# Kernel optimization log

Hardware: AMD Instinct MI355X
Metric: run time of the kernel (lower is better)

The kernel has to match this reference:

```python
import jax, jax.numpy as jnp
import numpy as np

HEAD_DIM = 64
NUM_FEATURES = 256


def _sample_orf(head_dim, num_features, seed=0):
    """Orthogonal random features with chi(d)-norm row scaling (FAVOR+)."""
    rng = np.random.RandomState(seed)
    blocks = []
    while len(blocks) * head_dim < num_features:
        G = rng.randn(head_dim, head_dim).astype(np.float32)
        Q, _ = np.linalg.qr(G)
        norms = np.linalg.norm(rng.randn(head_dim, head_dim).astype(np.float32), axis=1)
        blocks.append(np.diag(norms) @ Q.T)
    return np.concatenate(blocks, axis=0)[:num_features].astype(np.float32)


def _phi(x, omega, is_query):
    """FAVOR+ positive feature map with max-subtraction stabilization."""
    m = omega.shape[0]
    proj = jnp.einsum('bhnd,md->bhnm', x, omega)          # [B,H,N,M]
    norm = 0.5 * jnp.sum(x * x, axis=-1, keepdims=True)    # [B,H,N,1]
    log_phi = proj - norm
    if is_query:
        log_phi = log_phi - jnp.max(log_phi, axis=-1, keepdims=True)
    else:
        log_phi = log_phi - jnp.max(log_phi)
    return jnp.exp(log_phi) / np.float32(np.sqrt(m)) + 1e-4


def _causal_scan(phi_q, phi_k, v):
    """Causal linear-attention recurrence via lax.scan. States: S[B,H,M,D], z[B,H,M]."""
    B, H, N, M = phi_q.shape
    D = v.shape[-1]
    # seq-first for scan: [N,B,H,*]
    pq = jnp.moveaxis(phi_q, 2, 0)
    pk = jnp.moveaxis(phi_k, 2, 0)
    vt = jnp.moveaxis(v, 2, 0)

    S0 = jnp.zeros((B, H, M, D), dtype=phi_q.dtype)
    z0 = jnp.zeros((B, H, M), dtype=phi_q.dtype)

    def step(carry, xs):
        S, z = carry
        pq_i, pk_i, v_i = xs  # [B,H,M], [B,H,M], [B,H,D]
        S = S + pk_i[..., :, None] * v_i[..., None, :]
        z = z + pk_i
        num = jnp.einsum('bhm,bhmd->bhd', pq_i, S)
        den = jnp.sum(pq_i * z, axis=-1, keepdims=True) + 1e-6
        return (S, z), num / den

    _, out = jax.lax.scan(step, (S0, z0), (pq, pk, vt))  # out: [N,B,H,D]
    return jnp.moveaxis(out, 0, 2)


def setup_inputs() -> dict:
    key = jax.random.key(0)
    k1, k2, k3 = jax.random.split(key, 3)
    B, H, N, D = 2, 16, 4096, HEAD_DIM
    q = jax.random.normal(k1, (B, H, N, D), dtype=jnp.float32)
    k = jax.random.normal(k2, (B, H, N, D), dtype=jnp.float32)
    v = jax.random.normal(k3, (B, H, N, D), dtype=jnp.float32)
    omega = jnp.asarray(_sample_orf(HEAD_DIM, NUM_FEATURES))
    return {"q": q, "k": k, "v": v, "omega": omega}


def reference(q, k, v, omega):
    scale = q.shape[-1] ** (-0.25)
    phi_q = _phi(q * scale, omega, is_query=True)
    phi_k = _phi(k * scale, omega, is_query=False)
    # q_len == kv_len -> causal scan branch (matches original forward)
    out = _causal_scan(phi_q.astype(jnp.float32), phi_k.astype(jnp.float32),
                       v.astype(jnp.float32))
    return out.astype(q.dtype)
```

## Files before the change

kernel.cpp:

```cpp
#include <hip/hip_runtime.h>
#include <cstddef>

#define BH    32
#define NSEQ  4096
#define MFEAT 256
#define CHUNK 128
#define NCH   32
#define SROW  65
#define SPITCH (SROW*256)

#define SCALE 0.35355339059327373f

typedef unsigned int uint_t;
typedef _Float16 half_t;
typedef __attribute__((ext_vector_type(8))) _Float16 half8;
typedef __attribute__((ext_vector_type(4))) float f32x4;

__device__ __forceinline__ f32x4 mfma16(half8 a, half8 b, f32x4 c) {
  return __builtin_amdgcn_mfma_f32_16x16x32_f16(a, b, c, 0, 0, 0);
}
__device__ __forceinline__ uint_t enc_f(float x) {
  uint_t u = __float_as_uint(x);
  return (u & 0x80000000u) ? ~u : (u | 0x80000000u);
}
__device__ __forceinline__ float dec_f(uint_t u) {
  u = (u & 0x80000000u) ? (u ^ 0x80000000u) : ~u;
  return __uint_as_float(u);
}
__device__ __forceinline__ half8 cvt_h8(float4 a, float4 b) {
  half8 h;
  h[0] = (half_t)a.x; h[1] = (half_t)a.y; h[2] = (half_t)a.z; h[3] = (half_t)a.w;
  h[4] = (half_t)b.x; h[5] = (half_t)b.y; h[6] = (half_t)b.z; h[7] = (half_t)b.w;
  return h;
}

__global__ void k_init(uint_t* kmax) { *kmax = enc_f(-__builtin_inff()); }

__global__ __launch_bounds__(256, 2) void k_phi1(
    const float* __restrict__ q, const float* __restrict__ kx,
    const float* __restrict__ omega, uint_t* __restrict__ kmax,
    half_t* __restrict__ phiQ, float* __restrict__ hnKg)
{
  __shared__ half_t Wl[256 * 64];
  __shared__ float nrm[64];
  __shared__ float red[4];

  const int tid = threadIdx.x;
  const int lane = tid & 63;
  const int w = tid >> 6;
  const int lc = lane & 15, rg = lane >> 4, koff = rg * 8;
  const int swz = (lc & 7) << 3;
  const bool qpath = (blockIdx.x < 2048);
  const size_t rowbase = (size_t)(qpath ? blockIdx.x : (blockIdx.x - 2048)) * 64;

  for (int l = tid; l < 2048; l += 256) {
    int m = l >> 3, d8 = (l & 7) * 8;
    float4 a = *(const float4*)(omega + m * 64 + d8);
    float4 b = *(const float4*)(omega + m * 64 + d8 + 4);
    *(half8*)&Wl[m * 64 + (d8 ^ ((m & 7) << 3))] = cvt_h8(a, b);
  }

  if (qpath) {
    half8 aq[2];
    {
      const float* qp = q + (rowbase + w * 16 + lc) * 64 + koff;
      #pragma unroll
      for (int ks = 0; ks < 2; ks++) {
        float4 a = *(const float4*)(qp + ks * 32);
        float4 b = *(const float4*)(qp + ks * 32 + 4);
        a.x *= SCALE; a.y *= SCALE; a.z *= SCALE; a.w *= SCALE;
        b.x *= SCALE; b.y *= SCALE; b.z *= SCALE; b.w *= SCALE;
        aq[ks] = cvt_h8(a, b);
      }
    }
    __syncthreads();
    f32x4 acc[16];
    #pragma unroll
    for (int ct = 0; ct < 16; ct++) acc[ct] = (f32x4){0.f, 0.f, 0.f, 0.f};
    #pragma unroll
    for (int ks = 0; ks < 2; ks++)
      #pragma unroll
      for (int ct = 0; ct < 16; ct++) {
        half8 b = *(const half8*)&Wl[(ct * 16 + lc) * 64 + ((ks * 32 + koff) ^ swz)];
        acc[ct] = mfma16(aq[ks], b, acc[ct]);
      }
    float rowm[4];
    #pragma unroll
    for (int r = 0; r < 4; r++) {
      float m0 = -3.4e38f;
      #pragma unroll
      for (int ct = 0; ct < 16; ct++) m0 = fmaxf(m0, acc[ct][r]);
      m0 = fmaxf(m0, __shfl_xor(m0, 1, 64));
      m0 = fmaxf(m0, __shfl_xor(m0, 2, 64));
      m0 = fmaxf(m0, __shfl_xor(m0, 4, 64));
      m0 = fmaxf(m0, __shfl_xor(m0, 8, 64));
      rowm[r] = m0;
    }
    #pragma unroll
    for (int ct = 0; ct < 16; ct++)
      #pragma unroll
      for (int r = 0; r < 4; r++)
        acc[ct][r] = __expf(acc[ct][r] - rowm[r]) * 0.0625f + 1e-4f;

    half_t* st = Wl;
    #pragma unroll
    for (int hh = 0; hh < 2; hh++) {
      __syncthreads();
      #pragma unroll
      for (int c8 = 0; c8 < 8; c8++)
        #pragma unroll
        for (int r = 0; r < 4; r++)
          st[(w * 16 + rg * 4 + r) * 136 + c8 * 16 + lc] = (half_t)acc[hh * 8 + c8][r];
      __syncthreads();
      #pragma unroll
      for (int e = 0; e < 4; e++) {
        int l = tid + e * 256;
        int row = l >> 4, c = (l & 15) * 8;
        *(half8*)(phiQ + (rowbase + row) * 256 + hh * 128 + c) =
            *(const half8*)&st[row * 136 + c];
      }
    }
  } else {
    half8 akf[2];
    {
      const float* kp = kx + (rowbase + w * 16 + lc) * 64 + koff;
      float pn = 0.f;
      #pragma unroll
      for (int ks = 0; ks < 2; ks++) {
        float4 c = *(const float4*)(kp + ks * 32);
        float4 d = *(const float4*)(kp + ks * 32 + 4);
        c.x *= SCALE; c.y *= SCALE; c.z *= SCALE; c.w *= SCALE;
        d.x *= SCALE; d.y *= SCALE; d.z *= SCALE; d.w *= SCALE;
        pn += c.x * c.x + c.y * c.y + c.z * c.z + c.w * c.w
            + d.x * d.x + d.y * d.y + d.z * d.z + d.w * d.w;
        akf[ks] = cvt_h8(c, d);
      }
      pn += __shfl_xor(pn, 16, 64);
      pn += __shfl_xor(pn, 32, 64);
      if (rg == 0) {
        nrm[w * 16 + lc] = 0.5f * pn;
        hnKg[rowbase + w * 16 + lc] = 0.5f * pn;
      }
    }
    __syncthreads();
    f32x4 acc[16];
    #pragma unroll
    for (int ct = 0; ct < 16; ct++) acc[ct] = (f32x4){0.f, 0.f, 0.f, 0.f};
    #pragma unroll
    for (int ks = 0; ks < 2; ks++)
      #pragma unroll
      for (int ct = 0; ct < 16; ct++) {
        half8 b = *(const half8*)&Wl[(ct * 16 + lc) * 64 + ((ks * 32 + koff) ^ swz)];
        acc[ct] = mfma16(akf[ks], b, acc[ct]);
      }
    float hn[4];
    #pragma unroll
    for (int r = 0; r < 4; r++) hn[r] = nrm[w * 16 + rg * 4 + r];
    float bm = -3.4e38f;
    #pragma unroll
    for (int ct = 0; ct < 16; ct++)
      #pragma unroll
      for (int r = 0; r < 4; r++) bm = fmaxf(bm, acc[ct][r] - hn[r]);
    #pragma unroll
    for (int off = 1; off < 64; off <<= 1) bm = fmaxf(bm, __shfl_xor(bm, off, 64));
    if (lane == 0) red[w] = bm;
    __syncthreads();
    if (tid == 0)
      atomicMax(kmax, enc_f(fmaxf(fmaxf(red[0], red[1]), fmaxf(red[2], red[3]))));
  }
}

__global__ __launch_bounds__(256, 2) void k_state5(
    const float* __restrict__ kx, const float* __restrict__ v,
    const float* __restrict__ omega, const float* __restrict__ hnKg,
    const uint_t* __restrict__ kmax, half_t* __restrict__ spA,
    half_t* __restrict__ phiKg)
{
  __shared__ half_t sm[18432];
  half_t* Wl  = sm;
  half_t* pkT = sm;
  half_t* PhS = sm;
  half_t* vt  = sm + 8192;

  const int tid = threadIdx.x;
  const int lane = tid & 63;
  const int w = tid >> 6;
  const int lc = lane & 15, rg = lane >> 4, koff = rg * 8;
  const int wr = w * 32;
  const int swz = (lc & 7) << 3;
  const int mh = blockIdx.x & 1;
  const int blk = blockIdx.x >> 1;
  const size_t nbase = (size_t)(blk >> 5) * NSEQ + (size_t)(blk & 31) * CHUNK;
  const float gmaxv = dec_f(*kmax);

  for (int l = tid; l < 1024; l += 256) {
    int m = l >> 3, d8 = (l & 7) * 8;
    const float* op = omega + (mh * 128 + m) * 64 + d8;
    float4 a = *(const float4*)(op);
    float4 b = *(const float4*)(op + 4);
    *(half8*)&Wl[m * 64 + (d8 ^ ((m & 7) << 3))] = cvt_h8(a, b);
  }
  for (int l = tid; l < 2048; l += 256) {
    int j = l >> 4, dq = (l & 15) * 4;
    float4 vv = *(const float4*)(v + (nbase + j) * 64 + dq);
    vt[(dq + 0) * 128 + (j ^ (((dq + 0) & 7) << 3))] = (half_t)vv.x;
    vt[(dq + 1) * 128 + (j ^ (((dq + 1) & 7) << 3))] = (half_t)vv.y;
    vt[(dq + 2) * 128 + (j ^ (((dq + 2) & 7) << 3))] = (half_t)vv.z;
    vt[(dq + 3) * 128 + (j ^ (((dq + 3) & 7) << 3))] = (half_t)vv.w;
  }
  if (tid < 128) vt[64 * 128 + tid] = (half_t)1.0f;

  half8 ak[2][2];
  float hnr[2][4];
  #pragma unroll
  for (int rt = 0; rt < 2; rt++) {
    const float* kp = kx + (nbase + wr + rt * 16 + lc) * 64 + koff;
    #pragma unroll
    for (int ks = 0; ks < 2; ks++) {
      float4 a = *(const float4*)(kp + ks * 32);
      float4 b = *(const float4*)(kp + ks * 32 + 4);
      a.x *= SCALE; a.y *= SCALE; a.z *= SCALE; a.w *= SCALE;
      b.x *= SCALE; b.y *= SCALE; b.z *= SCALE; b.w *= SCALE;
      ak[rt][ks] = cvt_h8(a, b);
    }
    #pragma unroll
    for (int r = 0; r < 4; r++)
      hnr[rt][r] = hnKg[nbase + wr + rt * 16 + rg * 4 + r];
  }
  __syncthreads();

  f32x4 accP[2][8];
  #pragma unroll
  for (int rt = 0; rt < 2; rt++)
    #pragma unroll
    for (int ct = 0; ct < 8; ct++) accP[rt][ct] = (f32x4){0.f, 0.f, 0.f, 0.f};
  #pragma unroll
  for (int ks = 0; ks < 2; ks++)
    #pragma unroll
    for (int ct = 0; ct < 8; ct++) {
      half8 b = *(const half8*)&Wl[(ct * 16 + lc) * 64 + ((ks * 32 + koff) ^ swz)];
      accP[0][ct] = mfma16(ak[0][ks], b, accP[0][ct]);
      accP[1][ct] = mfma16(ak[1][ks], b, accP[1][ct]);
    }
  #pragma unroll
  for (int rt = 0; rt < 2; rt++)
    #pragma unroll
    for (int ct = 0; ct < 8; ct++)
      #pragma unroll
      for (int r = 0; r < 4; r++)
        accP[rt][ct][r] = __expf(accP[rt][ct][r] - hnr[rt][r] - gmaxv) * 0.0625f + 1e-4f;

  #pragma unroll
  for (int ms = 0; ms < 2; ms++) {
    __syncthreads();
    #pragma unroll
    for (int rt = 0; rt < 2; rt++)
      #pragma unroll
      for (int c4 = 0; c4 < 4; c4++) {
        int msub = c4 * 16 + lc;
        int ct = ms * 4 + c4;
        #pragma unroll
        for (int r = 0; r < 4; r++) {
          int j = wr + rt * 16 + rg * 4 + r;
          pkT[msub * 128 + (j ^ ((msub & 7) << 3))] = (half_t)accP[rt][ct][r];
        }
      }
    __syncthreads();
    f32x4 acc2[5];
    #pragma unroll
    for (int rt = 0; rt < 5; rt++) acc2[rt] = (f32x4){0.f, 0.f, 0.f, 0.f};
    #pragma unroll
    for (int ks = 0; ks < 4; ks++) {
      half8 b = *(const half8*)&pkT[(w * 16 + lc) * 128 + ((ks * 32 + koff) ^ swz)];
      #pragma unroll
      for (int rt = 0; rt < 5; rt++) {
        half8 a = *(const half8*)&vt[(rt * 16 + lc) * 128 + ((ks * 32 + koff) ^ swz)];
        acc2[rt] = mfma16(a, b, acc2[rt]);
      }
    }
    #pragma unroll
    for (int rt = 0; rt < 5; rt++)
      #pragma unroll
      for (int r = 0; r < 4; r++) {
        int row = rt * 16 + rg * 4 + r;
        if (row < SROW)
          spA[(size_t)blk * SPITCH + row * 256 + mh * 128 + ms * 64 + w * 16 + lc] =
              (half_t)acc2[rt][r];
      }
  }

  #pragma unroll
  for (int ms = 0; ms < 2; ms++) {
    __syncthreads();
    #pragma unroll
    for (int rt = 0; rt < 2; rt++)
      #pragma unroll
      for (int c4 = 0; c4 < 4; c4++)
        #pragma unroll
        for (int r = 0; r < 4; r++) {
          int j = wr + rt * 16 + rg * 4 + r;
          int msub = c4 * 16 + lc;
          PhS[j * 64 + (msub ^ ((j & 7) << 3))] = (half_t)accP[rt][ms * 4 + c4][r];
        }
    __syncthreads();
    #pragma unroll
    for (int e = 0; e < 4; e++) {
      int l = tid + e * 256;
      int j = l >> 3, c8 = (l & 7) * 8;
      *(half8*)(phiKg + (nbase + j) * 256 + mh * 128 + ms * 64 + c8) =
          *(const half8*)&PhS[j * 64 + (c8 ^ ((j & 7) << 3))];
    }
  }
}

__global__ __launch_bounds__(256) void k_prefix(
    const uint_t* __restrict__ spA, uint_t* __restrict__ spB)
{
  int r = blockIdx.x * 256 + threadIdx.x;
  if (r >= SPITCH / 2) return;
  int bh = blockIdx.y;
  const uint_t* src = spA + (size_t)bh * NCH * (SPITCH / 2) + r;
  uint_t* dst = spB + (size_t)bh * NCH * (SPITCH / 2) + r;
  float r0 = 0.f, r1 = 0.f;
  for (int c = 0; c < NCH; c++) {
    union { uint_t u; half_t h[2]; } cv, ov;
    cv.u = src[(size_t)c * (SPITCH / 2)];
    ov.h[0] = (half_t)r0; ov.h[1] = (half_t)r1;
    dst[(size_t)c * (SPITCH / 2)] = ov.u;
    r0 += (float)cv.h[0];
    r1 += (float)cv.h[1];
  }
}

__global__ __launch_bounds__(512) void k_attn8(
    const half_t* __restrict__ phiQ, const half_t* __restrict__ phiK,
    const float* __restrict__ v, const half_t* __restrict__ spB,
    float* __restrict__ out)
{
  __shared__ half_t sm[18432];
  half_t* PQ  = sm;
  half_t* SST = sm + 8192;
  half_t* AS  = sm;
  half_t* VT  = sm + 8192;

  const int tid = threadIdx.x;
  const int lane = tid & 63;
  const int w = tid >> 6;
  const int lc = lane & 15, rg = lane >> 4, koff = rg * 8;
  const int blk = blockIdx.x;
  const size_t nbase = (size_t)(blk >> 5) * NSEQ + (size_t)(blk & 31) * CHUNK;
  const half_t* spb = spB + (size_t)blk * SPITCH;
  const int swz = (lc & 7) << 3;

  f32x4 accA[8], accO[5];
  #pragma unroll
  for (int it = 0; it < 8; it++) accA[it] = (f32x4){0.f, 0.f, 0.f, 0.f};
  #pragma unroll
  for (int cs = 0; cs < 5; cs++) accO[cs] = (f32x4){0.f, 0.f, 0.f, 0.f};

  for (int mt = 0; mt < 4; mt++) {
    if (mt) __syncthreads();
    #pragma unroll
    for (int e = 0; e < 2; e++) {
      int l = tid + e * 512;
      int ro = l >> 3, c8 = (l & 7) * 8;
      *(half8*)&PQ[ro * 64 + (c8 ^ ((ro & 7) << 3))] =
          *(const half8*)(phiQ + (nbase + ro) * 256 + mt * 64 + c8);
    }
    { int ro = tid >> 3, c8 = (tid & 7) * 8;
      if (tid < 520)
        *(half8*)&SST[ro * 64 + (c8 ^ ((ro & 7) << 3))] =
            *(const half8*)(spb + ro * 256 + mt * 64 + c8); }
    if (tid < 8) { int l = tid + 512; int ro = l >> 3, c8 = (l & 7) * 8;
      *(half8*)&SST[ro * 64 + (c8 ^ ((ro & 7) << 3))] =
          *(const half8*)(spb + ro * 256 + mt * 64 + c8); }
    half8 af0 = *(const half8*)(phiK + (nbase + w * 16 + lc) * 256 + mt * 64 + koff);
    half8 af1 = *(const half8*)(phiK + (nbase + w * 16 + lc) * 256 + mt * 64 + 32 + koff);
    __syncthreads();
    #pragma unroll
    for (int ks2 = 0; ks2 < 64; ks2 += 32) {
      half8 a = ks2 ? af1 : af0;
      int sA = (ks2 + koff) ^ swz;
      half8 bO = *(const half8*)&PQ[(w * 16 + lc) * 64 + sA];
      #pragma unroll
      for (int it = 0; it < 8; it++) {
        half8 b = *(const half8*)&PQ[(it * 16 + lc) * 64 + sA];
        accA[it] = mfma16(a, b, accA[it]);
      }
      #pragma unroll
      for (int cs = 0; cs < 5; cs++) {
        half8 as_ = *(const half8*)&SST[(cs * 16 + lc) * 64 + sA];
        accO[cs] = mfma16(as_, bO, accO[cs]);
      }
    }
  }
  __syncthreads();

  #pragma unroll
  for (int e = 0; e < 4; e++) {
    int l = tid + e * 512;
    int j = l >> 4, dq = (l & 15) * 4;
    float4 vv = *(const float4*)(v + (nbase + j) * 64 + dq);
    VT[(dq + 0) * 128 + (j ^ (((dq + 0) & 7) << 3))] = (half_t)vv.x;
    VT[(dq + 1) * 128 + (j ^ (((dq + 1) & 7) << 3))] = (half_t)vv.y;
    VT[(dq + 2) * 128 + (j ^ (((dq + 2) & 7) << 3))] = (half_t)vv.z;
    VT[(dq + 3) * 128 + (j ^ (((dq + 3) & 7) << 3))] = (half_t)vv.w;
  }
  if (tid < 128) VT[64 * 128 + tid] = (half_t)1.0f;

  #pragma unroll
  for (int h = 0; h < 2; h++) {
    if ((w >> 2) == h) {
      #pragma unroll
      for (int it = 0; it < 8; it++) {
        int i = it * 16 + lc;
        #pragma unroll
        for (int r = 0; r < 4; r++) {
          int j = w * 16 + rg * 4 + r;
          float val = (j <= i) ? accA[it][r] : 0.f;
          AS[i * 64 + ((j - h * 64) ^ ((i & 7) << 3))] = (half_t)val;
        }
      }
    }
    __syncthreads();
    #pragma unroll
    for (int ks2 = 0; ks2 < 64; ks2 += 32) {
      int sj = (ks2 + koff) ^ swz;
      half8 b = *(const half8*)&AS[(w * 16 + lc) * 64 + sj];
      #pragma unroll
      for (int cs = 0; cs < 5; cs++) {
        half8 a = *(const half8*)&VT[(cs * 16 + lc) * 128 + ((h * 64 + ks2 + koff) ^ swz)];
        accO[cs] = mfma16(a, b, accO[cs]);
      }
    }
    __syncthreads();
  }

  float den = __shfl(accO[4][0], lane & 15, 64) + 1e-6f;
  float inv = 1.0f / den;
  float* OS = (float*)sm;
  #pragma unroll
  for (int cs = 0; cs < 4; cs++)
    #pragma unroll
    for (int r = 0; r < 4; r++)
      OS[(w * 16 + lc) * 68 + cs * 16 + rg * 4 + r] = accO[cs][r] * inv;
  __syncthreads();
  #pragma unroll
  for (int e = 0; e < 4; e++) {
    int l = tid + e * 512;
    int row = l >> 4, c4 = (l & 15) * 4;
    *(float4*)(out + (nbase + row) * 64 + c4) = *(const float4*)&OS[row * 68 + c4];
  }
}

extern "C" void kernel_launch(void* const* d_in, const int* in_sizes, int n_in,
                              void* d_out, int out_size, void* d_ws, size_t ws_size,
                              hipStream_t stream) {
  const float* q = (const float*)d_in[0];
  const float* k = (const float*)d_in[1];
  const float* v = (const float*)d_in[2];
  const float* omega = (const float*)d_in[3];
  float* out = (float*)d_out;
  char* ws = (char*)d_ws;

  float*  hnKg = (float*)(ws + 0);
  half_t* spB  = (half_t*)(ws + 524288);
  half_t* phiQ = (half_t*)(ws + 34603008);
  half_t* phiK = (half_t*)(ws + 101711872);
  half_t* spA  = (half_t*)(ws + 168820736);
  uint_t* kmax = (uint_t*)(ws + 202899456);

  k_init<<<1, 1, 0, stream>>>(kmax);
  k_phi1<<<4096, 256, 0, stream>>>(q, k, omega, kmax, phiQ, hnKg);
  k_state5<<<2048, 256, 0, stream>>>(k, v, omega, hnKg, kmax, spA, phiK);
  k_prefix<<<dim3(33, 32), 256, 0, stream>>>((const uint_t*)spA, (uint_t*)spB);
  k_attn8<<<1024, 512, 0, stream>>>(phiQ, phiK, v, spB, out);
}
```

Baseline: 159.8 us.

## Split phi-K computation from chunk-state kernel and use per-wave staging buffers

The fused k_state5 kernel, which recomputed phi(K) and built per-chunk KV states, is split into k_phiK, which computes and writes phi(K), and k_state6, which reads phi(K) from global memory and forms the chunk states over four 64-feature quarters. The phi kernels now stage output through a private per-wave shared buffer instead of reusing Wl, which removes block-wide barriers. The hnKg buffer is dropped; the norm is recomputed with a shuffle. In exchange there is an extra kernel launch, and phi(K) is written and then read back again.

```diff
diff --git a/kernel.cpp b/kernel.cpp
--- a/kernel.cpp
+++ b/kernel.cpp
@@ -36,13 +36,13 @@
 
 __global__ void k_init(uint_t* kmax) { *kmax = enc_f(-__builtin_inff()); }
 
-__global__ __launch_bounds__(256, 2) void k_phi1(
+__global__ __launch_bounds__(256, 2) void k_phi1b(
     const float* __restrict__ q, const float* __restrict__ kx,
     const float* __restrict__ omega, uint_t* __restrict__ kmax,
-    half_t* __restrict__ phiQ, float* __restrict__ hnKg)
+    half_t* __restrict__ phiQ)
 {
   __shared__ half_t Wl[256 * 64];
-  __shared__ float nrm[64];
+  __shared__ half_t st[4 * 16 * 136];
   __shared__ float red[4];
 
   const int tid = threadIdx.x;
@@ -102,45 +102,39 @@
       for (int r = 0; r < 4; r++)
         acc[ct][r] = __expf(acc[ct][r] - rowm[r]) * 0.0625f + 1e-4f;
 
-    half_t* st = Wl;
+    half_t* sw = st + w * 16 * 136;
     #pragma unroll
     for (int hh = 0; hh < 2; hh++) {
-      __syncthreads();
       #pragma unroll
       for (int c8 = 0; c8 < 8; c8++)
         #pragma unroll
         for (int r = 0; r < 4; r++)
-          st[(w * 16 + rg * 4 + r) * 136 + c8 * 16 + lc] = (half_t)acc[hh * 8 + c8][r];
-      __syncthreads();
+          sw[(rg * 4 + r) * 136 + c8 * 16 + lc] = (half_t)acc[hh * 8 + c8][r];
       #pragma unroll
       for (int e = 0; e < 4; e++) {
-        int l = tid + e * 256;
+        int l = lane + e * 64;
         int row = l >> 4, c = (l & 15) * 8;
-        *(half8*)(phiQ + (rowbase + row) * 256 + hh * 128 + c) =
-            *(const half8*)&st[row * 136 + c];
+        *(half8*)(phiQ + (rowbase + w * 16 + row) * 256 + hh * 128 + c) =
+            *(const half8*)&sw[row * 136 + c];
       }
     }
   } else {
     half8 akf[2];
+    float pnr = 0.f;
     {
       const float* kp = kx + (rowbase + w * 16 + lc) * 64 + koff;
-      float pn = 0.f;
       #pragma unroll
       for (int ks = 0; ks < 2; ks++) {
         float4 c = *(const float4*)(kp + ks * 32);
         float4 d = *(const float4*)(kp + ks * 32 + 4);
         c.x *= SCALE; c.y *= SCALE; c.z *= SCALE; c.w *= SCALE;
         d.x *= SCALE; d.y *= SCALE; d.z *= SCALE; d.w *= SCALE;
-        pn += c.x * c.x + c.y * c.y + c.z * c.z + c.w * c.w
-            + d.x * d.x + d.y * d.y + d.z * d.z + d.w * d.w;
+        pnr += c.x * c.x + c.y * c.y + c.z * c.z + c.w * c.w
+             + d.x * d.x + d.y * d.y + d.z * d.z + d.w * d.w;
         akf[ks] = cvt_h8(c, d);
       }
-      pn += __shfl_xor(pn, 16, 64);
-      pn += __shfl_xor(pn, 32, 64);
-      if (rg == 0) {
-        nrm[w * 16 + lc] = 0.5f * pn;
-        hnKg[rowbase + w * 16 + lc] = 0.5f * pn;
-      }
+      pnr += __shfl_xor(pnr, 16, 64);
+      pnr += __shfl_xor(pnr, 32, 64);
     }
     __syncthreads();
     f32x4 acc[16];
@@ -153,14 +147,13 @@
         half8 b = *(const half8*)&Wl[(ct * 16 + lc) * 64 + ((ks * 32 + koff) ^ swz)];
         acc[ct] = mfma16(akf[ks], b, acc[ct]);
       }
-    float hn[4];
-    #pragma unroll
-    for (int r = 0; r < 4; r++) hn[r] = nrm[w * 16 + rg * 4 + r];
     float bm = -3.4e38f;
     #pragma unroll
-    for (int ct = 0; ct < 16; ct++)
-      #pragma unroll
-      for (int r = 0; r < 4; r++) bm = fmaxf(bm, acc[ct][r] - hn[r]);
+    for (int r = 0; r < 4; r++) {
+      float hn = 0.5f * __shfl(pnr, rg * 4 + r, 64);
+      #pragma unroll
+      for (int ct = 0; ct < 16; ct++) bm = fmaxf(bm, acc[ct][r] - hn);
+    }
     #pragma unroll
     for (int off = 1; off < 64; off <<= 1) bm = fmaxf(bm, __shfl_xor(bm, off, 64));
     if (lane == 0) red[w] = bm;
@@ -170,36 +163,98 @@
   }
 }
 
-__global__ __launch_bounds__(256, 2) void k_state5(
-    const float* __restrict__ kx, const float* __restrict__ v,
-    const float* __restrict__ omega, const float* __restrict__ hnKg,
-    const uint_t* __restrict__ kmax, half_t* __restrict__ spA,
-    half_t* __restrict__ phiKg)
+__global__ __launch_bounds__(256, 2) void k_phiK(
+    const float* __restrict__ kx, const float* __restrict__ omega,
+    const uint_t* __restrict__ kmax, half_t* __restrict__ phiKg)
 {
-  __shared__ half_t sm[18432];
-  half_t* Wl  = sm;
-  half_t* pkT = sm;
-  half_t* PhS = sm;
-  half_t* vt  = sm + 8192;
+  __shared__ half_t Wl[256 * 64];
+  __shared__ half_t st[4 * 16 * 136];
 
   const int tid = threadIdx.x;
   const int lane = tid & 63;
   const int w = tid >> 6;
   const int lc = lane & 15, rg = lane >> 4, koff = rg * 8;
-  const int wr = w * 32;
   const int swz = (lc & 7) << 3;
-  const int mh = blockIdx.x & 1;
-  const int blk = blockIdx.x >> 1;
+  const size_t rowbase = (size_t)blockIdx.x * 64;
+  const float gmaxv = dec_f(*kmax);
+
+  for (int l = tid; l < 2048; l += 256) {
+    int m = l >> 3, d8 = (l & 7) * 8;
+    float4 a = *(const float4*)(omega + m * 64 + d8);
+    float4 b = *(const float4*)(omega + m * 64 + d8 + 4);
+    *(half8*)&Wl[m * 64 + (d8 ^ ((m & 7) << 3))] = cvt_h8(a, b);
+  }
+  half8 akf[2];
+  float pnr = 0.f;
+  {
+    const float* kp = kx + (rowbase + w * 16 + lc) * 64 + koff;
+    #pragma unroll
+    for (int ks = 0; ks < 2; ks++) {
+      float4 c = *(const float4*)(kp + ks * 32);
+      float4 d = *(const float4*)(kp + ks * 32 + 4);
+      c.x *= SCALE; c.y *= SCALE; c.z *= SCALE; c.w *= SCALE;
+      d.x *= SCALE; d.y *= SCALE; d.z *= SCALE; d.w *= SCALE;
+      pnr += c.x * c.x + c.y * c.y + c.z * c.z + c.w * c.w
+           + d.x * d.x + d.y * d.y + d.z * d.z + d.w * d.w;
+      akf[ks] = cvt_h8(c, d);
+    }
+    pnr += __shfl_xor(pnr, 16, 64);
+    pnr += __shfl_xor(pnr, 32, 64);
+  }
+  __syncthreads();
+
+  f32x4 acc[16];
+  #pragma unroll
+  for (int ct = 0; ct < 16; ct++) acc[ct] = (f32x4){0.f, 0.f, 0.f, 0.f};
+  #pragma unroll
+  for (int ks = 0; ks < 2; ks++)
+    #pragma unroll
+    for (int ct = 0; ct < 16; ct++) {
+      half8 b = *(const half8*)&Wl[(ct * 16 + lc) * 64 + ((ks * 32 + koff) ^ swz)];
+      acc[ct] = mfma16(akf[ks], b, acc[ct]);
+    }
+  float hn[4];
+  #pragma unroll
+  for (int r = 0; r < 4; r++) hn[r] = 0.5f * __shfl(pnr, rg * 4 + r, 64);
+  #pragma unroll
+  for (int ct = 0; ct < 16; ct++)
+    #pragma unroll
+    for (int r = 0; r < 4; r++)
+      acc[ct][r] = __expf(acc[ct][r] - hn[r] - gmaxv) * 0.0625f + 1e-4f;
+
+  half_t* sw = st + w * 16 * 136;
+  #pragma unroll
+  for (int hh = 0; hh < 2; hh++) {
+    #pragma unroll
+    for (int c8 = 0; c8 < 8; c8++)
+      #pragma unroll
+      for (int r = 0; r < 4; r++)
+        sw[(rg * 4 + r) * 136 + c8 * 16 + lc] = (half_t)acc[hh * 8 + c8][r];
+    #pragma unroll
+    for (int e = 0; e < 4; e++) {
+      int l = lane + e * 64;
+      int row = l >> 4, c = (l & 15) * 8;
+      *(half8*)(phiKg + (rowbase + w * 16 + row) * 256 + hh * 128 + c) =
+          *(const half8*)&sw[row * 136 + c];
+    }
+  }
+}
+
+__global__ __launch_bounds__(256, 2) void k_state6(
+    const float* __restrict__ v, const half_t* __restrict__ phiKg,
+    half_t* __restrict__ spA)
+{
+  __shared__ half_t vt[80 * 128];
+  __shared__ half_t pkT[64 * 136];
+
+  const int tid = threadIdx.x;
+  const int lane = tid & 63;
+  const int w = tid >> 6;
+  const int lc = lane & 15, rg = lane >> 4, koff = rg * 8;
+  const int mq = blockIdx.x & 3;
+  const int blk = blockIdx.x >> 2;
   const size_t nbase = (size_t)(blk >> 5) * NSEQ + (size_t)(blk & 31) * CHUNK;
-  const float gmaxv = dec_f(*kmax);
-
-  for (int l = tid; l < 1024; l += 256) {
-    int m = l >> 3, d8 = (l & 7) * 8;
-    const float* op = omega + (mh * 128 + m) * 64 + d8;
-    float4 a = *(const float4*)(op);
-    float4 b = *(const float4*)(op + 4);
-    *(half8*)&Wl[m * 64 + (d8 ^ ((m & 7) << 3))] = cvt_h8(a, b);
-  }
+
   for (int l = tid; l < 2048; l += 256) {
     int j = l >> 4, dq = (l & 15) * 4;
     float4 vv = *(const float4*)(v + (nbase + j) * 64 + dq);
@@ -210,107 +265,38 @@
   }
   if (tid < 128) vt[64 * 128 + tid] = (half_t)1.0f;
 
-  half8 ak[2][2];
-  float hnr[2][4];
-  #pragma unroll
-  for (int rt = 0; rt < 2; rt++) {
-    const float* kp = kx + (nbase + wr + rt * 16 + lc) * 64 + koff;
-    #pragma unroll
-    for (int ks = 0; ks < 2; ks++) {
-      float4 a = *(const float4*)(kp + ks * 32);
-      float4 b = *(const float4*)(kp + ks * 32 + 4);
-      a.x *= SCALE; a.y *= SCALE; a.z *= SCALE; a.w *= SCALE;
-      b.x *= SCALE; b.y *= SCALE; b.z *= SCALE; b.w *= SCALE;
-      ak[rt][ks] = cvt_h8(a, b);
-    }
-    #pragma unroll
-    for (int r = 0; r < 4; r++)
-      hnr[rt][r] = hnKg[nbase + wr + rt * 16 + rg * 4 + r];
+  #pragma unroll
+  for (int e = 0; e < 4; e++) {
+    int l = tid + e * 256;
+    int j = l >> 3, m8 = (l & 7) * 8;
+    half8 pk = *(const half8*)(phiKg + (nbase + j) * 256 + mq * 64 + m8);
+    #pragma unroll
+    for (int t = 0; t < 8; t++) pkT[(m8 + t) * 136 + j] = pk[t];
   }
   __syncthreads();
 
-  f32x4 accP[2][8];
-  #pragma unroll
-  for (int rt = 0; rt < 2; rt++)
-    #pragma unroll
-    for (int ct = 0; ct < 8; ct++) accP[rt][ct] = (f32x4){0.f, 0.f, 0.f, 0.f};
-  #pragma unroll
-  for (int ks = 0; ks < 2; ks++)
-    #pragma unroll
-    for (int ct = 0; ct < 8; ct++) {
-      half8 b = *(const half8*)&Wl[(ct * 16 + lc) * 64 + ((ks * 32 + koff) ^ swz)];
-      accP[0][ct] = mfma16(ak[0][ks], b, accP[0][ct]);
-      accP[1][ct] = mfma16(ak[1][ks], b, accP[1][ct]);
-    }
-  #pragma unroll
-  for (int rt = 0; rt < 2; rt++)
-    #pragma unroll
-    for (int ct = 0; ct < 8; ct++)
-      #pragma unroll
-      for (int r = 0; r < 4; r++)
-        accP[rt][ct][r] = __expf(accP[rt][ct][r] - hnr[rt][r] - gmaxv) * 0.0625f + 1e-4f;
-
-  #pragma unroll
-  for (int ms = 0; ms < 2; ms++) {
-    __syncthreads();
-    #pragma unroll
-    for (int rt = 0; rt < 2; rt++)
-      #pragma unroll
-      for (int c4 = 0; c4 < 4; c4++) {
-        int msub = c4 * 16 + lc;
-        int ct = ms * 4 + c4;
-        #pragma unroll
-        for (int r = 0; r < 4; r++) {
-          int j = wr + rt * 16 + rg * 4 + r;
-          pkT[msub * 128 + (j ^ ((msub & 7) << 3))] = (half_t)accP[rt][ct][r];
-        }
-      }
-    __syncthreads();
-    f32x4 acc2[5];
-    #pragma unroll
-    for (int rt = 0; rt < 5; rt++) acc2[rt] = (f32x4){0.f, 0.f, 0.f, 0.f};
-    #pragma unroll
-    for (int ks = 0; ks < 4; ks++) {
-      half8 b = *(const half8*)&pkT[(w * 16 + lc) * 128 + ((ks * 32 + koff) ^ swz)];
-      #pragma unroll
-      for (int rt = 0; rt < 5; rt++) {
-        half8 a = *(const half8*)&vt[(rt * 16 + lc) * 128 + ((ks * 32 + koff) ^ swz)];
-        acc2[rt] = mfma16(a, b, acc2[rt]);
-      }
-    }
-    #pragma unroll
-    for (int rt = 0; rt < 5; rt++)
-      #pragma unroll
-      for (int r = 0; r < 4; r++) {
-        int row = rt * 16 + rg * 4 + r;
-        if (row < SROW)
-          spA[(size_t)blk * SPITCH + row * 256 + mh * 128 + ms * 64 + w * 16 + lc] =
-              (half_t)acc2[rt][r];
-      }
-  }
-
-  #pragma unroll
-  for (int ms = 0; ms < 2; ms++) {
-    __syncthreads();
-    #pragma unroll
-    for (int rt = 0; rt < 2; rt++)
-      #pragma unroll
-      for (int c4 = 0; c4 < 4; c4++)
-        #pragma unroll
-        for (int r = 0; r < 4; r++) {
-          int j = wr + rt * 16 + rg * 4 + r;
-          int msub = c4 * 16 + lc;
-          PhS[j * 64 + (msub ^ ((j & 7) << 3))] = (half_t)accP[rt][ms * 4 + c4][r];
-        }
-    __syncthreads();
-    #pragma unroll
-    for (int e = 0; e < 4; e++) {
-      int l = tid + e * 256;
-      int j = l >> 3, c8 = (l & 7) * 8;
-      *(half8*)(phiKg + (nbase + j) * 256 + mh * 128 + ms * 64 + c8) =
-          *(const half8*)&PhS[j * 64 + (c8 ^ ((j & 7) << 3))];
-    }
-  }
+  f32x4 acc2[5];
+  #pragma unroll
+  for (int rt = 0; rt < 5; rt++) acc2[rt] = (f32x4){0.f, 0.f, 0.f, 0.f};
+  #pragma unroll
+  for (int ks = 0; ks < 4; ks++) {
+    half8 b = *(const half8*)&pkT[(w * 16 + lc) * 136 + ks * 32 + koff];
+    #pragma unroll
+    for (int rt = 0; rt < 5; rt++) {
+      int row = rt * 16 + lc;
+      half8 a = *(const half8*)&vt[row * 128 + ((ks * 32 + koff) ^ ((row & 7) << 3))];
+      acc2[rt] = mfma16(a, b, acc2[rt]);
+    }
+  }
+  #pragma unroll
+  for (int rt = 0; rt < 5; rt++)
+    #pragma unroll
+    for (int r = 0; r < 4; r++) {
+      int row = rt * 16 + rg * 4 + r;
+      if (row < SROW)
+        spA[(size_t)blk * SPITCH + row * 256 + mq * 64 + w * 16 + lc] =
+            (half_t)acc2[rt][r];
+    }
 }
 
 __global__ __launch_bounds__(256) void k_prefix(
@@ -463,16 +449,16 @@
   float* out = (float*)d_out;
   char* ws = (char*)d_ws;
 
-  float*  hnKg = (float*)(ws + 0);
-  half_t* spB  = (half_t*)(ws + 524288);
-  half_t* phiQ = (half_t*)(ws + 34603008);
-  half_t* phiK = (half_t*)(ws + 101711872);
-  half_t* spA  = (half_t*)(ws + 168820736);
-  uint_t* kmax = (uint_t*)(ws + 202899456);
+  half_t* spB  = (half_t*)(ws + 0);
+  half_t* phiQ = (half_t*)(ws + 34078720);
+  half_t* phiK = (half_t*)(ws + 101187584);
+  half_t* spA  = (half_t*)(ws + 168296448);
+  uint_t* kmax = (uint_t*)(ws + 202375168);
 
   k_init<<<1, 1, 0, stream>>>(kmax);
-  k_phi1<<<4096, 256, 0, stream>>>(q, k, omega, kmax, phiQ, hnKg);
-  k_state5<<<2048, 256, 0, stream>>>(k, v, omega, hnKg, kmax, spA, phiK);
+  k_phi1b<<<4096, 256, 0, stream>>>(q, k, omega, kmax, phiQ);
+  k_phiK<<<2048, 256, 0, stream>>>(k, omega, kmax, phiK);
+  k_state6<<<4096, 256, 0, stream>>>(v, phiK, spA);
   k_prefix<<<dim3(33, 32), 256, 0, stream>>>((const uint_t*)spA, (uint_t*)spB);
   k_attn8<<<1024, 512, 0, stream>>>(phiQ, phiK, v, spB, out);
 }
```

After: 178.5 us. 11.7% more time.
